# Kernel optimization log

Hardware: AMD Instinct MI355X
Metric: run time of the kernel (lower is better)

The kernel has to match this reference:

```python
import jax, jax.numpy as jnp
import numpy as np

DIM, HID = 32, 128
B, H, W = 2, 64, 64

def conv2d(x, w, b=None, pad=0, groups=1):
    out = jax.lax.conv_general_dilated(x, w, (1, 1), [(pad, pad), (pad, pad)],
        dimension_numbers=('NCHW', 'OIHW', 'NCHW'), feature_group_count=groups)
    if b is not None:
        out = out + b[None, :, None, None]
    return out

def gelu(x):
    return jax.nn.gelu(x, approximate=False)  # torch nn.GELU default (erf)

def s_conv(x, dw_w, dw_b, pw_w, pw_b):
    # separable conv: depthwise 3x3 (pad 1) then pointwise 1x1
    y = conv2d(x, dw_w, dw_b, pad=1, groups=x.shape[1])
    return conv2d(y, pw_w, pw_b, pad=0)

def deform_conv2d(x, off_w, off_b, w, b, k, pad):
    # torchvision-style deformable conv, stride 1, zero-padded bilinear sampling
    Bb, C, Hh, Ww = x.shape
    T = k * k
    off = conv2d(x, off_w, off_b, pad=pad).reshape(Bb, T, 2, Hh, Ww)
    dy, dx = off[:, :, 0], off[:, :, 1]                    # [B,T,H,W]
    ky, kx = jnp.meshgrid(jnp.arange(k), jnp.arange(k), indexing='ij')
    py = (jnp.arange(Hh, dtype=x.dtype).reshape(1, 1, Hh, 1)
          + ky.reshape(1, T, 1, 1).astype(x.dtype) - pad + dy)
    px = (jnp.arange(Ww, dtype=x.dtype).reshape(1, 1, 1, Ww)
          + kx.reshape(1, T, 1, 1).astype(x.dtype) - pad + dx)
    y0 = jnp.floor(py); x0 = jnp.floor(px)
    wy = py - y0; wx = px - x0
    y0 = y0.astype(jnp.int32); x0 = x0.astype(jnp.int32)
    flat = x.reshape(Bb, C, Hh * Ww)

    def corner(yi, xi, wgt):
        valid = (yi >= 0) & (yi < Hh) & (xi >= 0) & (xi < Ww)
        idx = jnp.clip(yi, 0, Hh - 1) * Ww + jnp.clip(xi, 0, Ww - 1)
        idx = jnp.broadcast_to(idx.reshape(Bb, 1, T * Hh * Ww), (Bb, C, T * Hh * Ww))
        v = jnp.take_along_axis(flat, idx, axis=2).reshape(Bb, C, T, Hh, Ww)
        return v * jnp.where(valid, wgt, jnp.zeros_like(wgt))[:, None]

    val = (corner(y0, x0, (1 - wy) * (1 - wx)) + corner(y0, x0 + 1, (1 - wy) * wx)
           + corner(y0 + 1, x0, wy * (1 - wx)) + corner(y0 + 1, x0 + 1, wy * wx))
    out = jnp.einsum('bcthw,oct->bohw', val, w.reshape(w.shape[0], C, T))
    return out + b[None, :, None, None]


def setup_inputs() -> dict:
    key = jax.random.key(0)
    ks = iter(jax.random.split(key, 40))
    def rn(shape, scale):
        return jax.random.normal(next(ks), shape, jnp.float32) * scale
    p = {}
    p['x'] = rn((B, H * W, DIM), 1.0)
    p['w1'] = rn((DIM, HID), DIM ** -0.5); p['b1'] = rn((HID,), 0.02)
    p['sc1_dw_w'] = rn((HID, 1, 3, 3), 1.0 / 3.0); p['sc1_dw_b'] = rn((HID,), 0.02)
    p['sc1_pw_w'] = rn((2 * HID, HID, 1, 1), HID ** -0.5); p['sc1_pw_b'] = rn((2 * HID,), 0.02)
    for name, k in (('d3', 7), ('d4', 3), ('d5', 5)):
        p[name + '_off_w'] = rn((2 * k * k, HID, k, k), 0.01 * (HID * k * k) ** -0.5)
        p[name + '_off_b'] = jnp.zeros((2 * k * k,), jnp.float32)
        p[name + '_w'] = rn((HID, HID, k, k), (HID * k * k) ** -0.5)
        p[name + '_b'] = rn((HID,), 0.02)
    p['w2'] = rn((HID, DIM), HID ** -0.5); p['b2'] = rn((DIM,), 0.02)
    return p


def reference(x, w1, b1, sc1_dw_w, sc1_dw_b, sc1_pw_w, sc1_pw_b,
              d3_off_w, d3_off_b, d3_w, d3_b,
              d4_off_w, d4_off_b, d4_w, d4_b,
              d5_off_w, d5_off_b, d5_w, d5_b, w2, b2):
    Bb, HW, C = x.shape
    hh = int(round(HW ** 0.5))
    x1 = gelu(x @ w1 + b1)                                   # [B,HW,HID]
    xi = x1.transpose(0, 2, 1).reshape(Bb, HID, hh, hh)       # b (h w) c -> b c h w
    y = gelu(s_conv(xi, sc1_dw_w, sc1_dw_b, sc1_pw_w, sc1_pw_b))  # [B,2*HID,h,w]
    a, g = jnp.split(y, 2, axis=1)
    a = gelu(deform_conv2d(a, d3_off_w, d3_off_b, d3_w, d3_b, 7, 3))
    a = gelu(deform_conv2d(a, d4_off_w, d4_off_b, d4_w, d4_b, 3, 1))
    a = gelu(deform_conv2d(a, d5_off_w, d5_off_b, d5_w, d5_b, 5, 2))
    z = gelu(a) * g                                           # gated GELU fusion
    z = z.reshape(Bb, HID, HW).transpose(0, 2, 1)             # b c h w -> b (h w) c
    return z @ w2 + b2
```

## Files before the change

kernel.cpp:

```cpp
#include <hip/hip_runtime.h>
#include <hip/hip_bf16.h>

#define HWSZ 4096

typedef _Float16 half8 __attribute__((ext_vector_type(8)));
typedef _Float16 half4 __attribute__((ext_vector_type(4)));
typedef float f32x4 __attribute__((ext_vector_type(4)));

__device__ __forceinline__ float gelu_f(float v) {
    return 0.5f * v * (1.0f + erff(v * 0.7071067811865475f));
}

__device__ __forceinline__ void wtr_elem(const float* __restrict__ w,
                                         _Float16* __restrict__ o,
                                         int i, int T, int Op, int O, float scale) {
    int c = i & 127;
    int op = (i >> 7) % Op;
    int t = i / (128 * Op);
    float v = (op < O) ? w[((size_t)(op * 128 + c)) * T + t] * scale : 0.f;
    o[i] = (_Float16)v;
}

__device__ __forceinline__ void wfrag_elemO(const float* __restrict__ w,
                                            _Float16* __restrict__ o,
                                            int i, int T, int MTt, int O, float scale) {
    int j = i & 7;
    int l = (i >> 3) & 63;
    int cc = (i >> 9) & 3;
    int m = (i >> 11) % MTt;
    int t = i / (2048 * MTt);
    int oc = m * 16 + (l & 15);
    int ch = (l >> 4) * 8 + cc * 32 + j;
    float v = (oc < O) ? w[((size_t)(oc * 128 + ch)) * T + t] * scale : 0.f;
    o[i] = (_Float16)v;
}

__global__ __launch_bounds__(256) void kprep(const float* __restrict__ dww,
                                             const float* __restrict__ pww,
                                             const float* __restrict__ o3w,
                                             const float* __restrict__ d3w,
                                             const float* __restrict__ o4w,
                                             const float* __restrict__ d4w,
                                             const float* __restrict__ o5w,
                                             const float* __restrict__ d5w,
                                             const float* __restrict__ w1,
                                             _Float16* __restrict__ dwt,
                                             _Float16* __restrict__ pwt,
                                             _Float16* __restrict__ wA3,
                                             _Float16* __restrict__ wA4,
                                             _Float16* __restrict__ wA5,
                                             _Float16* __restrict__ wM3,
                                             _Float16* __restrict__ wM4,
                                             _Float16* __restrict__ wM5,
                                             _Float16* __restrict__ wA1,
                                             unsigned int* __restrict__ zbase) {
    int i = blockIdx.x * 256 + threadIdx.x;
    if (i < 1152) {
        int c = i & 127, j = i >> 7;
        dwt[j * 128 + c] = (_Float16)dww[c * 9 + j];
        return;
    }
    i -= 1152;
    if (i < 32768) { pwt[i] = (_Float16)pww[i]; return; }
    i -= 32768;
    if (i < 802816) { wfrag_elemO(o3w, wA3, i, 49, 8, 98, 256.f); return; }
    i -= 802816;
    if (i < 36864) { wfrag_elemO(o4w, wA4, i, 9, 2, 18, 256.f); return; }
    i -= 36864;
    if (i < 204800) { wfrag_elemO(o5w, wA5, i, 25, 4, 50, 256.f); return; }
    i -= 204800;
    if (i < 802816) { wfrag_elemO(d3w, wM3, i, 49, 8, 128, 16.f); return; }
    i -= 802816;
    if (i < 147456) { wfrag_elemO(d4w, wM4, i, 9, 8, 128, 16.f); return; }
    i -= 147456;
    if (i < 409600) { wfrag_elemO(d5w, wM5, i, 25, 8, 128, 16.f); return; }
    i -= 409600;
    if (i < 4096) {
        int k = i & 31, oc = i >> 5;
        wA1[i] = (_Float16)w1[k * 128 + oc];
        return;
    }
    i -= 4096;
    if (i < 1290240) { zbase[i] = 0u; return; }
}

__global__ __launch_bounds__(512) void k1G(const float* __restrict__ x,
                                           const _Float16* __restrict__ wA1,
                                           const float* __restrict__ b1,
                                           _Float16* __restrict__ xicl) {
    int tid = threadIdx.x;
    int wv = tid >> 6;
    int l = tid & 63;
    int col = l & 15, kg = l >> 4;
    int blk = blockIdx.x;
    int b = blk >> 8;
    int p = ((blk & 255) << 4) + col;
    const float* xr = x + ((size_t)(b * HWSZ) + p) * 32 + kg * 8;
    half8 bf;
#pragma unroll
    for (int j = 0; j < 8; ++j) bf[j] = (_Float16)xr[j];
    half8 af = *(const half8*)(wA1 + (wv * 16 + col) * 32 + kg * 8);
    f32x4 acc = (f32x4){0.f, 0.f, 0.f, 0.f};
    acc = __builtin_amdgcn_mfma_f32_16x16x32_f16(af, bf, acc, 0, 0, 0);
    half4 t4;
#pragma unroll
    for (int r = 0; r < 4; ++r) {
        int oc = wv * 16 + kg * 4 + r;
        t4[r] = (_Float16)gelu_f(acc[r] + b1[oc]);
    }
    *(half4*)(xicl + ((size_t)(b * HWSZ) + p) * 128 + wv * 16 + kg * 4) = t4;
}

__global__ __launch_bounds__(256) void k2_cl(const _Float16* __restrict__ xicl,
                                             const _Float16* __restrict__ dwt,
                                             const float* __restrict__ dwb,
                                             _Float16* __restrict__ dcl) {
    int idx = blockIdx.x * 256 + threadIdx.x;
    int cg = idx & 15;
    int p = (idx >> 4) & 4095;
    int b = idx >> 16;
    int h = p >> 6, w = p & 63;
    const _Float16* base = xicl + (size_t)b * HWSZ * 128;
    float acc[8];
#pragma unroll
    for (int j = 0; j < 8; ++j) acc[j] = 0.f;
#pragma unroll
    for (int i = 0; i < 3; ++i) {
        int y = h + i - 1;
        if ((unsigned)y > 63u) continue;
#pragma unroll
        for (int j2 = 0; j2 < 3; ++j2) {
            int xx = w + j2 - 1;
            if ((unsigned)xx > 63u) continue;
            half8 v = *(const half8*)(base + ((size_t)(y * 64 + xx)) * 128 + cg * 8);
            half8 wv8 = *(const half8*)(dwt + (i * 3 + j2) * 128 + cg * 8);
#pragma unroll
            for (int j = 0; j < 8; ++j) acc[j] = fmaf((float)v[j], (float)wv8[j], acc[j]);
        }
    }
    half8 o;
#pragma unroll
    for (int j = 0; j < 8; ++j) o[j] = (_Float16)(acc[j] + dwb[cg * 8 + j]);
    *(half8*)(dcl + ((size_t)(b * HWSZ) + p) * 128 + cg * 8) = o;
}

__global__ __launch_bounds__(512) void k3G(const _Float16* __restrict__ dcl,
                                           const _Float16* __restrict__ pwt,
                                           const float* __restrict__ pwb,
                                           _Float16* __restrict__ clA,
                                           _Float16* __restrict__ gcl) {
    int tid = threadIdx.x;
    int wv = tid >> 6;
    int l = tid & 63;
    int col = l & 15, kg = l >> 4;
    int blk = blockIdx.x;
    int hf = blockIdx.y;
    int b = blk >> 8;
    int px0 = (blk & 255) << 4;
    int p = px0 + col;
    const _Float16* bp = dcl + ((size_t)(b * HWSZ) + p) * 128 + kg * 8;
    int oc0 = hf * 128 + wv * 16;
    const _Float16* ap = pwt + (size_t)(oc0 + col) * 128 + kg * 8;
    f32x4 acc = (f32x4){0.f, 0.f, 0.f, 0.f};
#pragma unroll
    for (int cc = 0; cc < 4; ++cc) {
        half8 bf = *(const half8*)(bp + cc * 32);
        half8 af = *(const half8*)(ap + cc * 32);
        acc = __builtin_amdgcn_mfma_f32_16x16x32_f16(af, bf, acc, 0, 0, 0);
    }
    int h = p >> 6, w = p & 63;
    half4 t4;
#pragma unroll
    for (int r = 0; r < 4; ++r) {
        int oc = oc0 + kg * 4 + r;
        t4[r] = (_Float16)gelu_f(acc[r] + pwb[oc]);
    }
    if (hf == 0) {
        _Float16* dst = clA + (size_t)b * 70 * 72 * 128 +
                        ((size_t)(h + 3) * 72 + (w + 3)) * 128 + wv * 16 + kg * 4;
        *(half4*)dst = t4;
    } else {
        *(half4*)(gcl + ((size_t)(b * HWSZ) + p) * 128 + wv * 16 + kg * 4) = t4;
    }
}

template <int KK, int PAD, int T, int MT, int NG, int NA, int WPX>
__global__ __launch_bounds__(512) void k4Gv4(const _Float16* __restrict__ cl,
                                             const _Float16* __restrict__ wA,
                                             const float* __restrict__ obias,
                                             float* __restrict__ offb, int OC) {
    constexpr int OCp = MT * 16;
    constexpr int COLS = WPX + KK - 1;
    constexpr int NB = 64 / WPX;
    __shared__ _Float16 bS[KK * COLS * 128];

    int tid = threadIdx.x;
    int blk = blockIdx.x;
    int w0 = (blk % NB) * WPX;
    int h = (blk / NB) & 63;
    int b = blk / (NB * 64);
    const _Float16* clb = cl + (size_t)b * 70 * 72 * 128;

    int hh0 = h + (3 - PAD);
    int ww0 = w0 + (3 - PAD);
    for (int g = tid; g < KK * COLS * 16; g += 512) {
        int r = g / (COLS * 16);
        int rest = g - r * (COLS * 16);
        int c = rest >> 4;
        int s = rest & 15;
        half8 v = *(const half8*)(clb + ((size_t)(hh0 + r) * 72 + (ww0 + c)) * 128 + s * 8);
        *(half8*)&bS[((r * COLS + c) * 16 + (s ^ (c & 7))) * 8] = v;
    }

    int wv = tid >> 6;
    int l = tid & 63;
    int col = l & 15, kg = l >> 4;
    int m = wv % MT;
    int ng = wv / MT;

    const half8* apb = (const half8*)wA + (size_t)m * 4 * 64 + l;
    half8 afv[4];
#pragma unroll
    for (int cc = 0; cc < 4; ++cc) afv[cc] = apb[cc * 64];

    f32x4 acc[NA];
#pragma unroll
    for (int a = 0; a < NA; ++a) acc[a] = (f32x4){0.f, 0.f, 0.f, 0.f};

    __syncthreads();

    for (int t = 0; t < T; ++t) {
        int ky = t / KK, kx = t - ky * KK;
        half8 afn[4];
        if (t + 1 < T) {
            const half8* apn = apb + (size_t)(t + 1) * MT * 4 * 64;
#pragma unroll
            for (int cc = 0; cc < 4; ++cc) afn[cc] = apn[cc * 64];
        }
#pragma unroll
        for (int a = 0; a < NA; ++a) {
            int cw = ng * NA * 16 + a * 16 + col + kx;
#pragma unroll
            for (int cc = 0; cc < 4; ++cc) {
                half8 bf = *(const half8*)&bS[((ky * COLS + cw) * 16 + ((cc * 4 + kg) ^ (cw & 7))) * 8];
                acc[a] = __builtin_amdgcn_mfma_f32_16x16x32_f16(afv[cc], bf, acc[a], 0, 0, 0);
            }
        }
#pragma unroll
        for (int cc = 0; cc < 4; ++cc) afv[cc] = afn[cc];
    }

#pragma unroll
    for (int a = 0; a < NA; ++a) {
        int px = h * 64 + w0 + ng * NA * 16 + a * 16 + col;
#pragma unroll
        for (int r = 0; r < 4; ++r) {
            int oc = m * 16 + kg * 4 + r;
            float v = acc[a][r] * (1.0f / 256.0f) + (oc < OC ? obias[oc] : 0.f);
            offb[((size_t)(b * OCp + oc)) * HWSZ + px] = v;
        }
    }
}

template <int KK, int PAD, int T, int OUTMODE>
__global__ __launch_bounds__(512, 4) void k5Gv14(const _Float16* __restrict__ cl,
                                                 const float* __restrict__ offb, int OFFP,
                                                 const _Float16* __restrict__ wM,
                                                 const float* __restrict__ bias,
                                                 _Float16* __restrict__ outH) {
    constexpr int ROWS = KK + 2;
    constexpr int COLSW = KK + 17;
    constexpr int UMAX = T * 16;
    __shared__ _Float16 win[ROWS * COLSW * 128];
    __shared__ _Float16 panel[2][16][128];
    __shared__ float pw4[4][UMAX];
    __shared__ uchar4 po4[UMAX];

    int tid = threadIdx.x;
    int blk = blockIdx.x;
    int b = blk >> 8;
    int px0 = (blk & 255) << 4;
    int h0 = px0 >> 6;
    int w0 = px0 & 63;
    const _Float16* clb = cl + (size_t)b * 70 * 72 * 128;
    const float* ob = offb + (size_t)b * OFFP * HWSZ;

    int R0 = min(max(h0 - PAD + 2, 0), 68 - KK);
    int C0 = min(max(w0 - PAD + 2, 0), 55 - KK);

    for (int g = tid; g < ROWS * COLSW * 16; g += 512) {
        int r = g / (COLSW * 16);
        int rest = g - r * (COLSW * 16);
        int c = rest >> 4, s = rest & 15;
        *(half8*)&win[((r * COLSW + c) << 7) + s * 8] =
            *(const half8*)(clb + ((size_t)(R0 + r) * 72 + (C0 + c)) * 128 + s * 8);
    }

    for (int q = tid; q < T * 16; q += 512) {
        int t = q >> 4;
        int px = q & 15;
        int p_s = px0 + px;
        int w_s = w0 + px;
        int ky = t / KK, kx = t - ky * KK;
        float dy = ob[(size_t)(2 * t) * HWSZ + p_s];
        float dx = ob[(size_t)(2 * t + 1) * HWSZ + p_s];
        float py = (float)(h0 + ky - PAD) + dy;
        float pxs = (float)(w_s + kx - PAD) + dx;
        float y0f = floorf(py), x0f = floorf(pxs);
        float wy = py - y0f, wx = pxs - x0f;
        int y0 = (int)y0f, x0 = (int)x0f;
        int y1 = y0 + 1, x1 = x0 + 1;
        bool vy0 = (y0 >= 0) && (y0 < 64), vy1 = (y1 >= 0) && (y1 < 64);
        bool vx0 = (x0 >= 0) && (x0 < 64), vx1 = (x1 >= 0) && (x1 < 64);
        int cy0 = min(max(y0, 0), 63) + 3, cy1 = min(max(y1, 0), 63) + 3;
        int cx0 = min(max(x0, 0), 63) + 3, cx1 = min(max(x1, 0), 63) + 3;
        pw4[0][q] = (vy0 && vx0) ? (1.f - wy) * (1.f - wx) : 0.f;
        pw4[1][q] = (vy0 && vx1) ? (1.f - wy) * wx : 0.f;
        pw4[2][q] = (vy1 && vx0) ? wy * (1.f - wx) : 0.f;
        pw4[3][q] = (vy1 && vx1) ? wy * wx : 0.f;
        po4[q] = make_uchar4((unsigned char)(cy0 - R0), (unsigned char)(cy1 - R0),
                             (unsigned char)(cx0 - C0), (unsigned char)(cx1 - C0));
    }

    int px_s = tid >> 5;
    int slice4 = tid & 31;
    int wv = tid >> 6;
    int l = tid & 63;
    int col = l & 15, kg = l >> 4;

    f32x4 acc = (f32x4){0.f, 0.f, 0.f, 0.f};
    half8 wA8[4], wB8[4];

    auto BLEND = [&](int t, int buf) {
        int q = t * 16 + px_s;
        _Float16 w00 = (_Float16)pw4[0][q], w01 = (_Float16)pw4[1][q];
        _Float16 w10 = (_Float16)pw4[2][q], w11 = (_Float16)pw4[3][q];
        uchar4 pk = po4[q];
        int o0 = ((int)pk.x * COLSW) << 7;
        int o1 = ((int)pk.y * COLSW) << 7;
        int o2 = ((int)pk.z) << 7;
        int o3 = ((int)pk.w) << 7;
        int c0 = slice4 * 4;
        half4 a00 = *(const half4*)(win + o0 + o2 + c0);
        half4 a01 = *(const half4*)(win + o0 + o3 + c0);
        half4 a10 = *(const half4*)(win + o1 + o2 + c0);
        half4 a11 = *(const half4*)(win + o1 + o3 + c0);
        half4 r = a00 * w00 + a01 * w01 + a10 * w10 + a11 * w11;
        *(half4*)&panel[buf][px_s][((slice4 >> 1) ^ (px_s & 7)) * 8 + (slice4 & 1) * 4] = r;
    };
    auto LOADW = [&](half8* w8, int t) {
        const half8* ap = (const half8*)wM + ((size_t)(t * 8 + wv) * 4) * 64 + l;
#pragma unroll
        for (int cc = 0; cc < 4; ++cc) w8[cc] = ap[cc * 64];
    };
    auto MM = [&](const half8* w8, int buf) {
#pragma unroll
        for (int cc = 0; cc < 4; ++cc) {
            half8 bf = *(const half8*)&panel[buf][col][((cc * 4 + kg) ^ (col & 7)) * 8];
            acc = __builtin_amdgcn_mfma_f32_16x16x32_f16(w8[cc], bf, acc, 0, 0, 0);
        }
    };
    auto BAR = [&]() {
        asm volatile("s_waitcnt lgkmcnt(0)" ::: "memory");
        __builtin_amdgcn_s_barrier();
        __builtin_amdgcn_sched_barrier(0);
    };

    LOADW(wA8, 0);
    if (1 < T) LOADW(wB8, 1);
    BAR();
    BLEND(0, 0);
    BAR();

    for (int t = 0; t < T; t += 2) {
        MM(wA8, t & 1);
        if (t + 2 < T) LOADW(wA8, t + 2);
        if (t + 1 < T) BLEND(t + 1, (t + 1) & 1);
        BAR();
        if (t + 1 < T) {
            MM(wB8, (t + 1) & 1);
            if (t + 3 < T) LOADW(wB8, t + 3);
            if (t + 2 < T) BLEND(t + 2, (t + 2) & 1);
            BAR();
        }
    }

    int p = px0 + col;
    half4 t4;
#pragma unroll
    for (int r = 0; r < 4; ++r) {
        int oc = wv * 16 + kg * 4 + r;
        t4[r] = (_Float16)gelu_f(acc[r] * (1.0f / 16.0f) + bias[oc]);
    }
    if (OUTMODE == 0) {
        int h = p >> 6, w = p & 63;
        _Float16* dst = outH + (size_t)b * 70 * 72 * 128 +
                        ((size_t)(h + 3) * 72 + (3 + w)) * 128 + wv * 16 + kg * 4;
        *(half4*)dst = t4;
    } else {
        *(half4*)(outH + ((size_t)(b * HWSZ) + p) * 128 + wv * 16 + kg * 4) = t4;
    }
}

__global__ __launch_bounds__(256) void k6z(const _Float16* __restrict__ a5cl,
                                           const _Float16* __restrict__ gcl,
                                           const float* __restrict__ w2,
                                           const float* __restrict__ b2,
                                           float* __restrict__ out) {
    __shared__ float zs[16][128];
    int tid = threadIdx.x;
    int blk = blockIdx.x;
    int b = blk >> 8;
    int px0 = (blk & 255) << 4;
    int px = tid >> 4, sl = tid & 15;
    size_t rb = ((size_t)(b * HWSZ) + px0 + px) * 128 + sl * 8;
    half8 a = *(const half8*)(a5cl + rb);
    half8 g = *(const half8*)(gcl + rb);
#pragma unroll
    for (int j = 0; j < 8; ++j)
        zs[px][sl * 8 + j] = gelu_f((float)a[j]) * (float)g[j];
    __syncthreads();
    int d2 = (tid & 15) * 2;
    float acc0 = b2[d2], acc1 = b2[d2 + 1];
#pragma unroll 16
    for (int c = 0; c < 128; ++c) {
        float zv = zs[px][c];
        acc0 = fmaf(zv, w2[c * 32 + d2], acc0);
        acc1 = fmaf(zv, w2[c * 32 + d2 + 1], acc1);
    }
    float* o = out + ((size_t)(b * HWSZ) + px0 + px) * 32 + d2;
    o[0] = acc0;
    o[1] = acc1;
}

extern "C" void kernel_launch(void* const* d_in, const int* in_sizes, int n_in,
                              void* d_out, int out_size, void* d_ws, size_t ws_size,
                              hipStream_t stream) {
    const float* x   = (const float*)d_in[0];
    const float* w1  = (const float*)d_in[1];
    const float* b1  = (const float*)d_in[2];
    const float* dww = (const float*)d_in[3];
    const float* dwb = (const float*)d_in[4];
    const float* pww = (const float*)d_in[5];
    const float* pwb = (const float*)d_in[6];
    const float* o3w = (const float*)d_in[7];
    const float* o3b = (const float*)d_in[8];
    const float* d3w = (const float*)d_in[9];
    const float* d3b = (const float*)d_in[10];
    const float* o4w = (const float*)d_in[11];
    const float* o4b = (const float*)d_in[12];
    const float* d4w = (const float*)d_in[13];
    const float* d4b = (const float*)d_in[14];
    const float* o5w = (const float*)d_in[15];
    const float* o5b = (const float*)d_in[16];
    const float* d5w = (const float*)d_in[17];
    const float* d5b = (const float*)d_in[18];
    const float* w2  = (const float*)d_in[19];
    const float* b2  = (const float*)d_in[20];

    float* ws = (float*)d_ws;
    float* offb = ws;
    _Float16* clA  = (_Float16*)(ws + 1048576);
    _Float16* clB  = (_Float16*)(ws + 1693696);
    _Float16* xicl = (_Float16*)(ws + 2338816);
    _Float16* dcl  = (_Float16*)(ws + 2863104);
    _Float16* gcl  = (_Float16*)(ws + 3387392);
    _Float16* a5cl = (_Float16*)(ws + 3911680);
    _Float16* wA3  = (_Float16*)(ws + 4960256);
    _Float16* wA4  = (_Float16*)(ws + 5361664);
    _Float16* wA5  = (_Float16*)(ws + 5380096);
    _Float16* wM3  = (_Float16*)(ws + 5482496);
    _Float16* wM4  = (_Float16*)(ws + 5883904);
    _Float16* wM5  = (_Float16*)(ws + 5957632);
    _Float16* dwt  = (_Float16*)(ws + 6162432);
    _Float16* pwt  = (_Float16*)(ws + 6163008);
    _Float16* wA1  = (_Float16*)(ws + 9325120);

    kprep<<<14581, 256, 0, stream>>>(dww, pww, o3w, d3w, o4w, d4w, o5w, d5w, w1,
                                     dwt, pwt, wA3, wA4, wA5, wM3, wM4, wM5, wA1,
                                     (unsigned int*)clA);

    k1G<<<512, 512, 0, stream>>>(x, wA1, b1, xicl);
    k2_cl<<<512, 256, 0, stream>>>(xicl, dwt, dwb, dcl);
    k3G<<<dim3(512, 2), 512, 0, stream>>>(dcl, pwt, pwb, clA, gcl);

    k4Gv4<7, 3, 49, 8, 1, 2, 32><<<256, 512, 0, stream>>>(clA, wA3, o3b, offb, 98);
    k5Gv14<7, 3, 49, 0><<<512, 512, 0, stream>>>(clA, offb, 128, wM3, d3b, clB);

    k4Gv4<3, 1, 9, 2, 4, 1, 64><<<128, 512, 0, stream>>>(clB, wA4, o4b, offb, 18);
    k5Gv14<3, 1, 9, 0><<<512, 512, 0, stream>>>(clB, offb, 32, wM4, d4b, clA);

    k4Gv4<5, 2, 25, 4, 2, 1, 32><<<256, 512, 0, stream>>>(clA, wA5, o5b, offb, 50);
    k5Gv14<5, 2, 25, 2><<<512, 512, 0, stream>>>(clA, offb, 64, wM5, d5b, a5cl);

    k6z<<<512, 256, 0, stream>>>(a5cl, gcl, w2, b2, (float*)d_out);
}
```

Before: 156.9 us.

## Use four-slot panel ring to halve barriers in deformable conv kernel

The blend/MFMA pipeline in the deformable conv kernel moves from a two-slot panel with one barrier per tap to a four-slot ring, doing two MFMA taps and two blends per barrier. Bilinear corner weights are stored as packed half4 instead of four float arrays, which cuts LDS reads and conversions inside the blend. The goal is fewer block-wide barriers and less LDS traffic per tap. In exchange it uses more shared memory, keeps more weight registers live, and the fp16 weights lose a little precision.

```diff
diff --git a/kernel.cpp b/kernel.cpp
--- a/kernel.cpp
+++ b/kernel.cpp
@@ -263,7 +263,7 @@
 }
 
 template <int KK, int PAD, int T, int OUTMODE>
-__global__ __launch_bounds__(512, 4) void k5Gv14(const _Float16* __restrict__ cl,
+__global__ __launch_bounds__(512, 4) void k5Gv15(const _Float16* __restrict__ cl,
                                                  const float* __restrict__ offb, int OFFP,
                                                  const _Float16* __restrict__ wM,
                                                  const float* __restrict__ bias,
@@ -272,8 +272,8 @@
     constexpr int COLSW = KK + 17;
     constexpr int UMAX = T * 16;
     __shared__ _Float16 win[ROWS * COLSW * 128];
-    __shared__ _Float16 panel[2][16][128];
-    __shared__ float pw4[4][UMAX];
+    __shared__ _Float16 panel[4][16][128];
+    __shared__ half4 pwh[UMAX];
     __shared__ uchar4 po4[UMAX];
 
     int tid = threadIdx.x;
@@ -314,10 +314,12 @@
         bool vx0 = (x0 >= 0) && (x0 < 64), vx1 = (x1 >= 0) && (x1 < 64);
         int cy0 = min(max(y0, 0), 63) + 3, cy1 = min(max(y1, 0), 63) + 3;
         int cx0 = min(max(x0, 0), 63) + 3, cx1 = min(max(x1, 0), 63) + 3;
-        pw4[0][q] = (vy0 && vx0) ? (1.f - wy) * (1.f - wx) : 0.f;
-        pw4[1][q] = (vy0 && vx1) ? (1.f - wy) * wx : 0.f;
-        pw4[2][q] = (vy1 && vx0) ? wy * (1.f - wx) : 0.f;
-        pw4[3][q] = (vy1 && vx1) ? wy * wx : 0.f;
+        half4 wq;
+        wq[0] = (_Float16)((vy0 && vx0) ? (1.f - wy) * (1.f - wx) : 0.f);
+        wq[1] = (_Float16)((vy0 && vx1) ? (1.f - wy) * wx : 0.f);
+        wq[2] = (_Float16)((vy1 && vx0) ? wy * (1.f - wx) : 0.f);
+        wq[3] = (_Float16)((vy1 && vx1) ? wy * wx : 0.f);
+        pwh[q] = wq;
         po4[q] = make_uchar4((unsigned char)(cy0 - R0), (unsigned char)(cy1 - R0),
                              (unsigned char)(cx0 - C0), (unsigned char)(cx1 - C0));
     }
@@ -331,10 +333,9 @@
     f32x4 acc = (f32x4){0.f, 0.f, 0.f, 0.f};
     half8 wA8[4], wB8[4];
 
-    auto BLEND = [&](int t, int buf) {
+    auto BLEND = [&](int t, int slot) {
         int q = t * 16 + px_s;
-        _Float16 w00 = (_Float16)pw4[0][q], w01 = (_Float16)pw4[1][q];
-        _Float16 w10 = (_Float16)pw4[2][q], w11 = (_Float16)pw4[3][q];
+        half4 wq = pwh[q];
         uchar4 pk = po4[q];
         int o0 = ((int)pk.x * COLSW) << 7;
         int o1 = ((int)pk.y * COLSW) << 7;
@@ -345,18 +346,18 @@
         half4 a01 = *(const half4*)(win + o0 + o3 + c0);
         half4 a10 = *(const half4*)(win + o1 + o2 + c0);
         half4 a11 = *(const half4*)(win + o1 + o3 + c0);
-        half4 r = a00 * w00 + a01 * w01 + a10 * w10 + a11 * w11;
-        *(half4*)&panel[buf][px_s][((slice4 >> 1) ^ (px_s & 7)) * 8 + (slice4 & 1) * 4] = r;
+        half4 r = a00 * wq[0] + a01 * wq[1] + a10 * wq[2] + a11 * wq[3];
+        *(half4*)&panel[slot][px_s][((slice4 >> 1) ^ (px_s & 7)) * 8 + (slice4 & 1) * 4] = r;
     };
     auto LOADW = [&](half8* w8, int t) {
         const half8* ap = (const half8*)wM + ((size_t)(t * 8 + wv) * 4) * 64 + l;
 #pragma unroll
         for (int cc = 0; cc < 4; ++cc) w8[cc] = ap[cc * 64];
     };
-    auto MM = [&](const half8* w8, int buf) {
+    auto MM = [&](const half8* w8, int slot) {
 #pragma unroll
         for (int cc = 0; cc < 4; ++cc) {
-            half8 bf = *(const half8*)&panel[buf][col][((cc * 4 + kg) ^ (col & 7)) * 8];
+            half8 bf = *(const half8*)&panel[slot][col][((cc * 4 + kg) ^ (col & 7)) * 8];
             acc = __builtin_amdgcn_mfma_f32_16x16x32_f16(w8[cc], bf, acc, 0, 0, 0);
         }
     };
@@ -370,19 +371,17 @@
     if (1 < T) LOADW(wB8, 1);
     BAR();
     BLEND(0, 0);
+    if (1 < T) BLEND(1, 1);
     BAR();
 
     for (int t = 0; t < T; t += 2) {
-        MM(wA8, t & 1);
+        MM(wA8, t & 3);
+        if (t + 1 < T) MM(wB8, (t + 1) & 3);
         if (t + 2 < T) LOADW(wA8, t + 2);
-        if (t + 1 < T) BLEND(t + 1, (t + 1) & 1);
+        if (t + 3 < T) LOADW(wB8, t + 3);
+        if (t + 2 < T) BLEND(t + 2, (t + 2) & 3);
+        if (t + 3 < T) BLEND(t + 3, (t + 3) & 3);
         BAR();
-        if (t + 1 < T) {
-            MM(wB8, (t + 1) & 1);
-            if (t + 3 < T) LOADW(wB8, t + 3);
-            if (t + 2 < T) BLEND(t + 2, (t + 2) & 1);
-            BAR();
-        }
     }
 
     int p = px0 + col;
@@ -485,13 +484,13 @@
     k3G<<<dim3(512, 2), 512, 0, stream>>>(dcl, pwt, pwb, clA, gcl);
 
     k4Gv4<7, 3, 49, 8, 1, 2, 32><<<256, 512, 0, stream>>>(clA, wA3, o3b, offb, 98);
-    k5Gv14<7, 3, 49, 0><<<512, 512, 0, stream>>>(clA, offb, 128, wM3, d3b, clB);
+    k5Gv15<7, 3, 49, 0><<<512, 512, 0, stream>>>(clA, offb, 128, wM3, d3b, clB);
 
     k4Gv4<3, 1, 9, 2, 4, 1, 64><<<128, 512, 0, stream>>>(clB, wA4, o4b, offb, 18);
-    k5Gv14<3, 1, 9, 0><<<512, 512, 0, stream>>>(clB, offb, 32, wM4, d4b, clA);
+    k5Gv15<3, 1, 9, 0><<<512, 512, 0, stream>>>(clB, offb, 32, wM4, d4b, clA);
 
     k4Gv4<5, 2, 25, 4, 2, 1, 32><<<256, 512, 0, stream>>>(clA, wA5, o5b, offb, 50);
-    k5Gv14<5, 2, 25, 2><<<512, 512, 0, stream>>>(clA, offb, 64, wM5, d5b, a5cl);
+    k5Gv15<5, 2, 25, 2><<<512, 512, 0, stream>>>(clA, offb, 64, wM5, d5b, a5cl);
 
     k6z<<<512, 256, 0, stream>>>(a5cl, gcl, w2, b2, (float*)d_out);
 }
```

After: 157.1 us. Within noise of the previous version (+0.1%).
